# Performance work log

Hardware: AMD Instinct MI355X
Metric: run time of the kernel (lower is better)

Reference implementation:

```python
import jax, jax.numpy as jnp
import numpy as np


def setup_inputs() -> dict:
    key = jax.random.key(0)
    ks = jax.random.split(key, 4)
    B, T, D, H, E = 4, 2048, 1024, 4096, 8
    s = 0.02
    x = jax.random.normal(ks[0], (B, T, D), dtype=jnp.float32)
    Wr = jax.random.normal(ks[1], (D, E), dtype=jnp.float32) * s
    br = jnp.zeros((E,), dtype=jnp.float32)
    W1 = jax.random.normal(ks[2], (E, D, H), dtype=jnp.float32) * s
    b1 = jnp.zeros((E, H), dtype=jnp.float32)
    W2 = jax.random.normal(ks[3], (E, H, D), dtype=jnp.float32) * s
    b2 = jnp.zeros((E, D), dtype=jnp.float32)
    return {"x": x, "Wr": Wr, "br": br, "W1": W1, "b1": b1, "W2": W2, "b2": b2}


def reference(x, Wr, br, W1, b1, W2, b2):
    # Router: top-1 selection
    logits = jnp.einsum('btd,de->bte', x, Wr) + br            # [B,T,E]
    probs = jax.nn.softmax(logits, axis=-1)                   # [B,T,E]
    expert_idx = jnp.argmax(probs, axis=-1)                   # [B,T] int
    E = W1.shape[0]
    onehot = jax.nn.one_hot(expert_idx, E, dtype=x.dtype)     # [B,T,E]
    # Dense grouped-MLP over all experts, then combine with one-hot routing.
    # h: [B,E,T,H]
    h = jax.nn.relu(jnp.einsum('btd,edh->beth', x, W1) + b1[None, :, None, :])
    y = jnp.einsum('beth,ehd->betd', h, W2) + b2[None, :, None, :]  # [B,E,T,D]
    out = jnp.einsum('bte,betd->btd', onehot, y)              # [B,T,D]
    return out, probs, expert_idx
```

## Files before the change

kernel.cpp:

```cpp
#include <hip/hip_runtime.h>

#define NTOK 8192
#define DD 1024
#define HH 4096
#define EE 8
#define MAXBLK 72

typedef __attribute__((ext_vector_type(8))) short bf16x8;
typedef __attribute__((ext_vector_type(4))) float f32x4;

__device__ __forceinline__ unsigned short f2bf(float f) {
  unsigned u = __builtin_bit_cast(unsigned, f);
  u += 0x7fffu + ((u >> 16) & 1u);
  return (unsigned short)(u >> 16);
}

union Pack8 {
  unsigned short u[8];
  uint4 v;
};

__device__ __forceinline__ void gload_lds16(const void* g, void* l) {
  __builtin_amdgcn_global_load_lds(
      (const __attribute__((address_space(1))) unsigned int*)g,
      (__attribute__((address_space(3))) unsigned int*)l, 16, 0, 0);
}

__global__ __launch_bounds__(256) void k_router(
    const float* __restrict__ x, const float* __restrict__ Wr,
    const float* __restrict__ br, float* __restrict__ probs,
    float* __restrict__ idxf, int* __restrict__ idxi) {
  const int lane = threadIdx.x & 63;
  const int token = blockIdx.x * 4 + (threadIdx.x >> 6);
  const float* xr = x + (size_t)token * DD;

  float acc[EE];
#pragma unroll
  for (int e = 0; e < EE; ++e) acc[e] = 0.f;

#pragma unroll
  for (int i = 0; i < 4; ++i) {
    const int d0 = i * 256 + lane * 4;
    const float4 xv = *reinterpret_cast<const float4*>(xr + d0);
    const float xs[4] = {xv.x, xv.y, xv.z, xv.w};
#pragma unroll
    for (int j = 0; j < 4; ++j) {
      const float xd = xs[j];
      const float4 w0 = *reinterpret_cast<const float4*>(Wr + (size_t)(d0 + j) * EE);
      const float4 w1 = *reinterpret_cast<const float4*>(Wr + (size_t)(d0 + j) * EE + 4);
      acc[0] += xd * w0.x; acc[1] += xd * w0.y; acc[2] += xd * w0.z; acc[3] += xd * w0.w;
      acc[4] += xd * w1.x; acc[5] += xd * w1.y; acc[6] += xd * w1.z; acc[7] += xd * w1.w;
    }
  }
#pragma unroll
  for (int s = 32; s > 0; s >>= 1) {
#pragma unroll
    for (int e = 0; e < EE; ++e) acc[e] += __shfl_xor(acc[e], s, 64);
  }

  float lg[EE];
#pragma unroll
  for (int e = 0; e < EE; ++e) lg[e] = acc[e] + br[e];

  int best = 0;
  float bv = lg[0];
#pragma unroll
  for (int e = 1; e < EE; ++e) {
    if (lg[e] > bv) { bv = lg[e]; best = e; }
  }
  float p[EE], s = 0.f;
#pragma unroll
  for (int e = 0; e < EE; ++e) { p[e] = expf(lg[e] - bv); s += p[e]; }
  const float inv = 1.f / s;

  if (lane == 0) {
#pragma unroll
    for (int e = 0; e < EE; ++e) probs[(size_t)token * EE + e] = p[e] * inv;
    idxf[token] = (float)best;
    idxi[token] = best;
  }
}

__global__ __launch_bounds__(512) void k_compact(const int* __restrict__ idxi,
                                                 int* __restrict__ cnt,
                                                 int* __restrict__ off,
                                                 int* __restrict__ sorted,
                                                 int* __restrict__ meta) {
  __shared__ int sidx[NTOK];
  __shared__ int scnt[EE], soff[EE];
  const int tid = threadIdx.x;
  for (int i = tid; i < NTOK; i += 512) sidx[i] = idxi[i];
  __syncthreads();
  const int w = tid >> 6, lane = tid & 63;
  if (w < EE) {
    int c = 0;
    for (int i = 0; i < NTOK / 64; ++i) {
      unsigned long long m = __ballot(sidx[i * 64 + lane] == w);
      c += __popcll(m);
    }
    if (lane == 0) scnt[w] = c;
  }
  __syncthreads();
  if (tid == 0) {
    int s = 0;
    for (int e = 0; e < EE; ++e) { soff[e] = s; s += scnt[e]; }
    int nb = 0;
    for (int e = 0; e < EE; ++e) {
      const int nmb = (scnt[e] + 127) >> 7;
      for (int m = 0; m < nmb; ++m) {
        meta[16 + nb] = e;
        meta[96 + nb] = m << 7;
        ++nb;
      }
    }
    meta[0] = nb;
  }
  __syncthreads();
  if (w < EE) {
    int base = soff[w];
    const unsigned long long ltmask = (1ull << lane) - 1ull;
    for (int i = 0; i < NTOK / 64; ++i) {
      const int tok = i * 64 + lane;
      const bool f = (sidx[tok] == w);
      unsigned long long m = __ballot(f);
      if (f) {
        int r = __popcll(m & ltmask);
        sorted[base + r] = tok;
      }
      base += __popcll(m);
    }
    if (lane == 0) { cnt[w] = scnt[w]; off[w] = soff[w]; }
  }
}

__global__ __launch_bounds__(256) void k_cvt_x(const float* __restrict__ x,
                                               unsigned short* __restrict__ xb) {
  const size_t i = ((size_t)blockIdx.x * 256 + threadIdx.x) * 8;
  const float4 a = *reinterpret_cast<const float4*>(x + i);
  const float4 b = *reinterpret_cast<const float4*>(x + i + 4);
  Pack8 p;
  p.u[0] = f2bf(a.x); p.u[1] = f2bf(a.y); p.u[2] = f2bf(a.z); p.u[3] = f2bf(a.w);
  p.u[4] = f2bf(b.x); p.u[5] = f2bf(b.y); p.u[6] = f2bf(b.z); p.u[7] = f2bf(b.w);
  *reinterpret_cast<uint4*>(xb + i) = p.v;
}

__global__ __launch_bounds__(256) void k_trcvt(const float* __restrict__ in,
                                               unsigned short* __restrict__ outp,
                                               int R, int C) {
  const int e = blockIdx.z;
  const float* src = in + (size_t)e * R * C;
  unsigned short* dst = outp + (size_t)e * R * C;
  __shared__ float t[32][33];
  const int r0 = blockIdx.y * 32, c0 = blockIdx.x * 32;
  const int tr = threadIdx.x >> 3, tc4 = (threadIdx.x & 7) * 4;
  const float4 v = *reinterpret_cast<const float4*>(src + (size_t)(r0 + tr) * C + c0 + tc4);
  t[tr][tc4 + 0] = v.x; t[tr][tc4 + 1] = v.y; t[tr][tc4 + 2] = v.z; t[tr][tc4 + 3] = v.w;
  __syncthreads();
  union { unsigned short u[4]; uint2 v2; } p;
#pragma unroll
  for (int j = 0; j < 4; ++j) p.u[j] = f2bf(t[tc4 + j][tr]);
  *reinterpret_cast<uint2*>(&dst[(size_t)(c0 + tr) * R + r0 + tc4]) = p.v2;
}

__global__ __launch_bounds__(256) void k_gemm1n(
    const unsigned short* __restrict__ xb, const unsigned short* __restrict__ W1t,
    const float* __restrict__ b1, const int* __restrict__ meta,
    const int* __restrict__ cnt, const int* __restrict__ off,
    const int* __restrict__ sorted, unsigned short* __restrict__ h) {
  const int bid = blockIdx.x;
  if (bid >= meta[0]) return;
  const int e = meta[16 + bid];
  const int m0 = meta[96 + bid];
  const int c = cnt[e], base = off[e];
  const int n0 = blockIdx.y * 128;

  __shared__ __align__(16) unsigned short Al[128 * 64];
  __shared__ __align__(16) unsigned short Bl[128 * 64];

  const int tid = threadIdx.x, l = tid & 63, w = tid >> 6;

  const unsigned short* aptr[4];
  const unsigned short* bptr[4];
  unsigned short* alds[4];
  unsigned short* blds[4];
#pragma unroll
  for (int i = 0; i < 4; ++i) {
    const int r = i * 32 + w * 8 + (l >> 3);
    const int swz = ((l & 7) ^ (r & 7)) * 8;
    int ar = m0 + r; if (ar >= c) ar = c - 1;
    const int tok = sorted[base + ar];
    aptr[i] = xb + (size_t)tok * DD + swz;
    bptr[i] = W1t + ((size_t)e * HH + n0 + r) * DD + swz;
    alds[i] = &Al[r * 64 + (l & 7) * 8];
    blds[i] = &Bl[r * 64 + (l & 7) * 8];
  }

  const int lr = l & 15, lg = l >> 4;
  const int wr = w >> 1, wc = w & 1;
  int aoff[4], bofr[4], aswz[4], bswz[4];
#pragma unroll
  for (int m = 0; m < 4; ++m) {
    int row = wr * 64 + m * 16 + lr;
    aoff[m] = row * 64; aswz[m] = row & 7;
    row = wc * 64 + m * 16 + lr;
    bofr[m] = row * 64; bswz[m] = row & 7;
  }

  f32x4 acc[4][4];
#pragma unroll
  for (int m = 0; m < 4; ++m)
#pragma unroll
    for (int n = 0; n < 4; ++n) acc[m][n] = {0.f, 0.f, 0.f, 0.f};

  for (int k0 = 0; k0 < DD; k0 += 64) {
    __syncthreads();
#pragma unroll
    for (int i = 0; i < 4; ++i) gload_lds16(aptr[i] + k0, alds[i]);
#pragma unroll
    for (int i = 0; i < 4; ++i) gload_lds16(bptr[i] + k0, blds[i]);
    __syncthreads();
#pragma unroll
    for (int ks = 0; ks < 2; ++ks) {
      bf16x8 af[4], bv[4];
#pragma unroll
      for (int m = 0; m < 4; ++m)
        af[m] = *reinterpret_cast<const bf16x8*>(&Al[aoff[m] + (((ks * 4 + lg) ^ aswz[m]) * 8)]);
#pragma unroll
      for (int n = 0; n < 4; ++n)
        bv[n] = *reinterpret_cast<const bf16x8*>(&Bl[bofr[n] + (((ks * 4 + lg) ^ bswz[n]) * 8)]);
#pragma unroll
      for (int m = 0; m < 4; ++m)
#pragma unroll
        for (int n = 0; n < 4; ++n)
          acc[m][n] = __builtin_amdgcn_mfma_f32_16x16x32_bf16(af[m], bv[n], acc[m][n], 0, 0, 0);
    }
  }

  const int valid = c - m0;
#pragma unroll
  for (int m = 0; m < 4; ++m) {
#pragma unroll
    for (int rr = 0; rr < 4; ++rr) {
      const int tr = wr * 64 + m * 16 + lg * 4 + rr;
      if (tr < valid) {
        const size_t row = (size_t)(base + m0 + tr);
#pragma unroll
        for (int n = 0; n < 4; ++n) {
          const int col = n0 + wc * 64 + n * 16 + lr;
          const float v = acc[m][n][rr] + b1[e * HH + col];
          h[row * HH + col] = f2bf(fmaxf(v, 0.f));
        }
      }
    }
  }
}

__global__ __launch_bounds__(256) void k_gemm2n(
    const unsigned short* __restrict__ h, const unsigned short* __restrict__ W2t,
    const float* __restrict__ b2, const int* __restrict__ meta,
    const int* __restrict__ cnt, const int* __restrict__ off,
    const int* __restrict__ sorted, float* __restrict__ out) {
  const int bid = blockIdx.x;
  if (bid >= meta[0]) return;
  const int e = meta[16 + bid];
  const int m0 = meta[96 + bid];
  const int c = cnt[e], base = off[e];
  const int n0 = blockIdx.y * 128;

  __shared__ __align__(16) unsigned short Al[128 * 64];
  __shared__ __align__(16) unsigned short Bl[128 * 64];

  const int tid = threadIdx.x, l = tid & 63, w = tid >> 6;

  const unsigned short* aptr[4];
  const unsigned short* bptr[4];
  unsigned short* alds[4];
  unsigned short* blds[4];
#pragma unroll
  for (int i = 0; i < 4; ++i) {
    const int r = i * 32 + w * 8 + (l >> 3);
    const int swz = ((l & 7) ^ (r & 7)) * 8;
    int ar = m0 + r; if (ar >= c) ar = c - 1;
    aptr[i] = h + (size_t)(base + ar) * HH + swz;
    bptr[i] = W2t + ((size_t)e * DD + n0 + r) * HH + swz;
    alds[i] = &Al[r * 64 + (l & 7) * 8];
    blds[i] = &Bl[r * 64 + (l & 7) * 8];
  }

  const int lr = l & 15, lg = l >> 4;
  const int wr = w >> 1, wc = w & 1;
  int aoff[4], bofr[4], aswz[4], bswz[4];
#pragma unroll
  for (int m = 0; m < 4; ++m) {
    int row = wr * 64 + m * 16 + lr;
    aoff[m] = row * 64; aswz[m] = row & 7;
    row = wc * 64 + m * 16 + lr;
    bofr[m] = row * 64; bswz[m] = row & 7;
  }

  f32x4 acc[4][4];
#pragma unroll
  for (int m = 0; m < 4; ++m)
#pragma unroll
    for (int n = 0; n < 4; ++n) acc[m][n] = {0.f, 0.f, 0.f, 0.f};

  for (int k0 = 0; k0 < HH; k0 += 64) {
    __syncthreads();
#pragma unroll
    for (int i = 0; i < 4; ++i) gload_lds16(aptr[i] + k0, alds[i]);
#pragma unroll
    for (int i = 0; i < 4; ++i) gload_lds16(bptr[i] + k0, blds[i]);
    __syncthreads();
#pragma unroll
    for (int ks = 0; ks < 2; ++ks) {
      bf16x8 af[4], bv[4];
#pragma unroll
      for (int m = 0; m < 4; ++m)
        af[m] = *reinterpret_cast<const bf16x8*>(&Al[aoff[m] + (((ks * 4 + lg) ^ aswz[m]) * 8)]);
#pragma unroll
      for (int n = 0; n < 4; ++n)
        bv[n] = *reinterpret_cast<const bf16x8*>(&Bl[bofr[n] + (((ks * 4 + lg) ^ bswz[n]) * 8)]);
#pragma unroll
      for (int m = 0; m < 4; ++m)
#pragma unroll
        for (int n = 0; n < 4; ++n)
          acc[m][n] = __builtin_amdgcn_mfma_f32_16x16x32_bf16(af[m], bv[n], acc[m][n], 0, 0, 0);
    }
  }

  const int valid = c - m0;
#pragma unroll
  for (int m = 0; m < 4; ++m) {
#pragma unroll
    for (int rr = 0; rr < 4; ++rr) {
      const int tr = wr * 64 + m * 16 + lg * 4 + rr;
      if (tr < valid) {
        const int token = sorted[base + m0 + tr];
#pragma unroll
        for (int n = 0; n < 4; ++n) {
          const int col = n0 + wc * 64 + n * 16 + lr;
          out[(size_t)token * DD + col] = acc[m][n][rr] + b2[e * DD + col];
        }
      }
    }
  }
}

#define BM 128
#define BN 128
#define BK 32
#define PAD 40

__global__ __launch_bounds__(256) void k_gemm1_f32(
    const float* __restrict__ x, const float* __restrict__ W1,
    const float* __restrict__ b1, const int* __restrict__ cnt,
    const int* __restrict__ off, const int* __restrict__ sorted,
    unsigned short* __restrict__ h) {
  const int e = blockIdx.x >> 6;
  const int mb = blockIdx.x & 63;
  const int n0 = blockIdx.y * BN;
  const int c = cnt[e];
  const int m0 = mb * BM;
  if (m0 >= c) return;
  const int base = off[e];

  __shared__ __align__(16) unsigned short Al[BM * PAD];
  __shared__ __align__(16) unsigned short Bl[BN * PAD];

  const int tid = threadIdx.x;
  const int ar = tid >> 1, ah = tid & 1;
  int arow = m0 + ar; if (arow >= c) arow = c - 1;
  const int atok = sorted[base + arow];
  const float* asrc = x + (size_t)atok * DD + ah * 16;
  const int bn = tid & 127, bkg = tid >> 7;
  const float* bsrc = W1 + (size_t)e * DD * HH + (size_t)(bkg * 16) * HH + n0 + bn;

  const int lane = tid & 63, w = tid >> 6;
  const int wr = w >> 1, wc = w & 1;
  const int lr = lane & 15, lg = lane >> 4;

  f32x4 acc[4][4];
#pragma unroll
  for (int m = 0; m < 4; ++m)
#pragma unroll
    for (int n = 0; n < 4; ++n) acc[m][n] = {0.f, 0.f, 0.f, 0.f};

  for (int k0 = 0; k0 < DD; k0 += BK) {
    Pack8 pa0, pa1;
    {
      const float* s4 = asrc + k0;
#pragma unroll
      for (int q = 0; q < 2; ++q) {
        float4 f = *reinterpret_cast<const float4*>(s4 + q * 4);
        pa0.u[q * 4 + 0] = f2bf(f.x); pa0.u[q * 4 + 1] = f2bf(f.y);
        pa0.u[q * 4 + 2] = f2bf(f.z); pa0.u[q * 4 + 3] = f2bf(f.w);
      }
#pragma unroll
      for (int q = 0; q < 2; ++q) {
        float4 f = *reinterpret_cast<const float4*>(s4 + 8 + q * 4);
        pa1.u[q * 4 + 0] = f2bf(f.x); pa1.u[q * 4 + 1] = f2bf(f.y);
        pa1.u[q * 4 + 2] = f2bf(f.z); pa1.u[q * 4 + 3] = f2bf(f.w);
      }
    }
    Pack8 pb0, pb1;
    {
      const float* bs = bsrc + (size_t)k0 * HH;
#pragma unroll
      for (int q = 0; q < 8; ++q) pb0.u[q] = f2bf(bs[(size_t)q * HH]);
#pragma unroll
      for (int q = 0; q < 8; ++q) pb1.u[q] = f2bf(bs[(size_t)(q + 8) * HH]);
    }
    __syncthreads();
    *reinterpret_cast<uint4*>(&Al[ar * PAD + ah * 16]) = pa0.v;
    *reinterpret_cast<uint4*>(&Al[ar * PAD + ah * 16 + 8]) = pa1.v;
    *reinterpret_cast<uint4*>(&Bl[bn * PAD + bkg * 16]) = pb0.v;
    *reinterpret_cast<uint4*>(&Bl[bn * PAD + bkg * 16 + 8]) = pb1.v;
    __syncthreads();

    bf16x8 af[4], bf[4];
#pragma unroll
    for (int m = 0; m < 4; ++m)
      af[m] = *reinterpret_cast<const bf16x8*>(&Al[(wr * 64 + m * 16 + lr) * PAD + lg * 8]);
#pragma unroll
    for (int n = 0; n < 4; ++n)
      bf[n] = *reinterpret_cast<const bf16x8*>(&Bl[(wc * 64 + n * 16 + lr) * PAD + lg * 8]);
#pragma unroll
    for (int m = 0; m < 4; ++m)
#pragma unroll
      for (int n = 0; n < 4; ++n)
        acc[m][n] = __builtin_amdgcn_mfma_f32_16x16x32_bf16(af[m], bf[n], acc[m][n], 0, 0, 0);
  }

  const int valid = c - m0;
#pragma unroll
  for (int m = 0; m < 4; ++m) {
#pragma unroll
    for (int r = 0; r < 4; ++r) {
      const int tr = wr * 64 + m * 16 + lg * 4 + r;
      if (tr < valid) {
        const size_t row = (size_t)(base + m0 + tr);
#pragma unroll
        for (int n = 0; n < 4; ++n) {
          const int col = n0 + wc * 64 + n * 16 + lr;
          float v = acc[m][n][r] + b1[e * HH + col];
          v = fmaxf(v, 0.f);
          h[row * HH + col] = f2bf(v);
        }
      }
    }
  }
}

__global__ __launch_bounds__(256) void k_gemm2_f32(
    const unsigned short* __restrict__ h, const float* __restrict__ W2,
    const float* __restrict__ b2, const int* __restrict__ cnt,
    const int* __restrict__ off, const int* __restrict__ sorted,
    float* __restrict__ out) {
  const int e = blockIdx.x >> 6;
  const int mb = blockIdx.x & 63;
  const int n0 = blockIdx.y * BN;
  const int c = cnt[e];
  const int m0 = mb * BM;
  if (m0 >= c) return;
  const int base = off[e];

  __shared__ __align__(16) unsigned short Al[BM * PAD];
  __shared__ __align__(16) unsigned short Bl[BN * PAD];

  const int tid = threadIdx.x;
  const int ar = tid >> 1, ah = tid & 1;
  int arow = m0 + ar; if (arow >= c) arow = c - 1;
  const unsigned short* asrc = h + (size_t)(base + arow) * HH + ah * 16;
  const int bn = tid & 127, bkg = tid >> 7;
  const float* bsrc = W2 + (size_t)e * HH * DD + (size_t)(bkg * 16) * DD + n0 + bn;

  const int lane = tid & 63, w = tid >> 6;
  const int wr = w >> 1, wc = w & 1;
  const int lr = lane & 15, lg = lane >> 4;

  f32x4 acc[4][4];
#pragma unroll
  for (int m = 0; m < 4; ++m)
#pragma unroll
    for (int n = 0; n < 4; ++n) acc[m][n] = {0.f, 0.f, 0.f, 0.f};

  for (int k0 = 0; k0 < HH; k0 += BK) {
    const uint4 a0 = *reinterpret_cast<const uint4*>(asrc + k0);
    const uint4 a1 = *reinterpret_cast<const uint4*>(asrc + k0 + 8);
    Pack8 pb0, pb1;
    {
      const float* bs = bsrc + (size_t)k0 * DD;
#pragma unroll
      for (int q = 0; q < 8; ++q) pb0.u[q] = f2bf(bs[(size_t)q * DD]);
#pragma unroll
      for (int q = 0; q < 8; ++q) pb1.u[q] = f2bf(bs[(size_t)(q + 8) * DD]);
    }
    __syncthreads();
    *reinterpret_cast<uint4*>(&Al[ar * PAD + ah * 16]) = a0;
    *reinterpret_cast<uint4*>(&Al[ar * PAD + ah * 16 + 8]) = a1;
    *reinterpret_cast<uint4*>(&Bl[bn * PAD + bkg * 16]) = pb0.v;
    *reinterpret_cast<uint4*>(&Bl[bn * PAD + bkg * 16 + 8]) = pb1.v;
    __syncthreads();

    bf16x8 af[4], bf[4];
#pragma unroll
    for (int m = 0; m < 4; ++m)
      af[m] = *reinterpret_cast<const bf16x8*>(&Al[(wr * 64 + m * 16 + lr) * PAD + lg * 8]);
#pragma unroll
    for (int n = 0; n < 4; ++n)
      bf[n] = *reinterpret_cast<const bf16x8*>(&Bl[(wc * 64 + n * 16 + lr) * PAD + lg * 8]);
#pragma unroll
    for (int m = 0; m < 4; ++m)
#pragma unroll
      for (int n = 0; n < 4; ++n)
        acc[m][n] = __builtin_amdgcn_mfma_f32_16x16x32_bf16(af[m], bf[n], acc[m][n], 0, 0, 0);
  }

  const int valid = c - m0;
#pragma unroll
  for (int m = 0; m < 4; ++m) {
#pragma unroll
    for (int r = 0; r < 4; ++r) {
      const int tr = wr * 64 + m * 16 + lg * 4 + r;
      if (tr < valid) {
        const int token = sorted[base + m0 + tr];
#pragma unroll
        for (int n = 0; n < 4; ++n) {
          const int col = n0 + wc * 64 + n * 16 + lr;
          out[(size_t)token * DD + col] = acc[m][n][r] + b2[e * DD + col];
        }
      }
    }
  }
}

extern "C" void kernel_launch(void* const* d_in, const int* in_sizes, int n_in,
                              void* d_out, int out_size, void* d_ws, size_t ws_size,
                              hipStream_t stream) {
  const float* x  = (const float*)d_in[0];
  const float* Wr = (const float*)d_in[1];
  const float* br = (const float*)d_in[2];
  const float* W1 = (const float*)d_in[3];
  const float* b1 = (const float*)d_in[4];
  const float* W2 = (const float*)d_in[5];
  const float* b2 = (const float*)d_in[6];

  float* out   = (float*)d_out;
  float* probs = out + (size_t)NTOK * DD;
  float* idxf  = probs + (size_t)NTOK * EE;

  char* ws = (char*)d_ws;
  int* cnt    = (int*)(ws + 0);
  int* off    = (int*)(ws + 64);
  int* meta   = (int*)(ws + 128);
  int* idxi   = (int*)(ws + 1024);
  int* sorted = (int*)(ws + 33792);

  const size_t OFF_XB  = 66560;
  const size_t OFF_W1T = OFF_XB + (size_t)NTOK * DD * 2;
  const size_t OFF_H   = OFF_W1T + (size_t)EE * DD * HH * 2;
  const size_t OFF_W2T = OFF_XB;
  const size_t NEED    = OFF_H + (size_t)NTOK * HH * 2;

  k_router<<<NTOK / 4, 256, 0, stream>>>(x, Wr, br, probs, idxf, idxi);
  k_compact<<<1, 512, 0, stream>>>(idxi, cnt, off, sorted, meta);

  if (ws_size >= NEED) {
    unsigned short* xb  = (unsigned short*)(ws + OFF_XB);
    unsigned short* W1t = (unsigned short*)(ws + OFF_W1T);
    unsigned short* W2t = (unsigned short*)(ws + OFF_W2T);
    unsigned short* h   = (unsigned short*)(ws + OFF_H);
    k_cvt_x<<<(NTOK * DD) / (256 * 8), 256, 0, stream>>>(x, xb);
    k_trcvt<<<dim3(HH / 32, DD / 32, EE), 256, 0, stream>>>(W1, W1t, DD, HH);
    k_gemm1n<<<dim3(MAXBLK, HH / 128), 256, 0, stream>>>(xb, W1t, b1, meta, cnt, off, sorted, h);
    k_trcvt<<<dim3(DD / 32, HH / 32, EE), 256, 0, stream>>>(W2, W2t, HH, DD);
    k_gemm2n<<<dim3(MAXBLK, DD / 128), 256, 0, stream>>>(h, W2t, b2, meta, cnt, off, sorted, out);
  } else {
    unsigned short* h = (unsigned short*)(ws + OFF_XB);
    k_gemm1_f32<<<dim3(EE * (NTOK / BM), HH / BN), 256, 0, stream>>>(x, W1, b1, cnt, off, sorted, h);
    k_gemm2_f32<<<dim3(EE * (NTOK / BM), DD / BN), 256, 0, stream>>>(h, W2, b2, cnt, off, sorted, out);
  }
}
```

Baseline: 400.7 us.

## Double-buffer GEMM LDS tiles, fuse x conversion into router, widen transpose tiles

Both grouped GEMMs now keep two LDS buffers and prefetch the next K-tile with global_load_lds while computing on the current one. Barriers use manual vmcnt waits so the global-load latency can overlap with MFMA work. The bf16 conversion of x moves into the router kernel, removing a separate pass over x, and the weight transpose-convert now uses 64x64 tiles that store bf16 in LDS and write 16-byte rows. The fp32 fallback path and its workspace-size check are removed, so the code assumes the workspace is large enough, and doubling LDS may lower occupancy.

```diff
diff --git a/kernel.cpp b/kernel.cpp
--- a/kernel.cpp
+++ b/kernel.cpp
@@ -5,6 +5,8 @@
 #define HH 4096
 #define EE 8
 #define MAXBLK 72
+#define NT1 16
+#define NT2 64
 
 typedef __attribute__((ext_vector_type(8))) short bf16x8;
 typedef __attribute__((ext_vector_type(4))) float f32x4;
@@ -29,7 +31,8 @@
 __global__ __launch_bounds__(256) void k_router(
     const float* __restrict__ x, const float* __restrict__ Wr,
     const float* __restrict__ br, float* __restrict__ probs,
-    float* __restrict__ idxf, int* __restrict__ idxi) {
+    float* __restrict__ idxf, int* __restrict__ idxi,
+    unsigned short* __restrict__ xb) {
   const int lane = threadIdx.x & 63;
   const int token = blockIdx.x * 4 + (threadIdx.x >> 6);
   const float* xr = x + (size_t)token * DD;
@@ -42,6 +45,10 @@
   for (int i = 0; i < 4; ++i) {
     const int d0 = i * 256 + lane * 4;
     const float4 xv = *reinterpret_cast<const float4*>(xr + d0);
+    union { unsigned short u[4]; uint2 v; } pk;
+    pk.u[0] = f2bf(xv.x); pk.u[1] = f2bf(xv.y);
+    pk.u[2] = f2bf(xv.z); pk.u[3] = f2bf(xv.w);
+    *reinterpret_cast<uint2*>(xb + (size_t)token * DD + d0) = pk.v;
     const float xs[4] = {xv.x, xv.y, xv.z, xv.w};
 #pragma unroll
     for (int j = 0; j < 4; ++j) {
@@ -133,33 +140,33 @@
   }
 }
 
-__global__ __launch_bounds__(256) void k_cvt_x(const float* __restrict__ x,
-                                               unsigned short* __restrict__ xb) {
-  const size_t i = ((size_t)blockIdx.x * 256 + threadIdx.x) * 8;
-  const float4 a = *reinterpret_cast<const float4*>(x + i);
-  const float4 b = *reinterpret_cast<const float4*>(x + i + 4);
-  Pack8 p;
-  p.u[0] = f2bf(a.x); p.u[1] = f2bf(a.y); p.u[2] = f2bf(a.z); p.u[3] = f2bf(a.w);
-  p.u[4] = f2bf(b.x); p.u[5] = f2bf(b.y); p.u[6] = f2bf(b.z); p.u[7] = f2bf(b.w);
-  *reinterpret_cast<uint4*>(xb + i) = p.v;
-}
-
-__global__ __launch_bounds__(256) void k_trcvt(const float* __restrict__ in,
-                                               unsigned short* __restrict__ outp,
-                                               int R, int C) {
+__global__ __launch_bounds__(256) void k_trcvt64(const float* __restrict__ in,
+                                                 unsigned short* __restrict__ outp,
+                                                 int R, int C) {
   const int e = blockIdx.z;
-  const float* src = in + (size_t)e * R * C;
-  unsigned short* dst = outp + (size_t)e * R * C;
-  __shared__ float t[32][33];
-  const int r0 = blockIdx.y * 32, c0 = blockIdx.x * 32;
-  const int tr = threadIdx.x >> 3, tc4 = (threadIdx.x & 7) * 4;
-  const float4 v = *reinterpret_cast<const float4*>(src + (size_t)(r0 + tr) * C + c0 + tc4);
-  t[tr][tc4 + 0] = v.x; t[tr][tc4 + 1] = v.y; t[tr][tc4 + 2] = v.z; t[tr][tc4 + 3] = v.w;
+  const int r0 = blockIdx.y * 64, c0 = blockIdx.x * 64;
+  const float* src = in + (size_t)e * R * C + (size_t)r0 * C + c0;
+  unsigned short* dst = outp + (size_t)e * R * C + (size_t)c0 * R + r0;
+  __shared__ unsigned short t[64 * 66];
+  const int tid = threadIdx.x;
+#pragma unroll
+  for (int it = 0; it < 4; ++it) {
+    const int r = it * 16 + (tid >> 4), c4 = (tid & 15) * 4;
+    const float4 v = *reinterpret_cast<const float4*>(src + (size_t)r * C + c4);
+    t[r * 66 + c4 + 0] = f2bf(v.x);
+    t[r * 66 + c4 + 1] = f2bf(v.y);
+    t[r * 66 + c4 + 2] = f2bf(v.z);
+    t[r * 66 + c4 + 3] = f2bf(v.w);
+  }
   __syncthreads();
-  union { unsigned short u[4]; uint2 v2; } p;
-#pragma unroll
-  for (int j = 0; j < 4; ++j) p.u[j] = f2bf(t[tc4 + j][tr]);
-  *reinterpret_cast<uint2*>(&dst[(size_t)(c0 + tr) * R + r0 + tc4]) = p.v2;
+#pragma unroll
+  for (int it = 0; it < 2; ++it) {
+    const int cc = it * 32 + (tid >> 3), r8 = (tid & 7) * 8;
+    Pack8 p;
+#pragma unroll
+    for (int j = 0; j < 8; ++j) p.u[j] = t[(r8 + j) * 66 + cc];
+    *reinterpret_cast<uint4*>(dst + (size_t)cc * R + r8) = p.v;
+  }
 }
 
 __global__ __launch_bounds__(256) void k_gemm1n(
@@ -174,15 +181,14 @@
   const int c = cnt[e], base = off[e];
   const int n0 = blockIdx.y * 128;
 
-  __shared__ __align__(16) unsigned short Al[128 * 64];
-  __shared__ __align__(16) unsigned short Bl[128 * 64];
+  __shared__ __align__(16) unsigned short Al[2][128 * 64];
+  __shared__ __align__(16) unsigned short Bl[2][128 * 64];
 
   const int tid = threadIdx.x, l = tid & 63, w = tid >> 6;
 
   const unsigned short* aptr[4];
   const unsigned short* bptr[4];
-  unsigned short* alds[4];
-  unsigned short* blds[4];
+  int soff4[4];
 #pragma unroll
   for (int i = 0; i < 4; ++i) {
     const int r = i * 32 + w * 8 + (l >> 3);
@@ -191,19 +197,18 @@
     const int tok = sorted[base + ar];
     aptr[i] = xb + (size_t)tok * DD + swz;
     bptr[i] = W1t + ((size_t)e * HH + n0 + r) * DD + swz;
-    alds[i] = &Al[r * 64 + (l & 7) * 8];
-    blds[i] = &Bl[r * 64 + (l & 7) * 8];
+    soff4[i] = r * 64 + (l & 7) * 8;
   }
 
   const int lr = l & 15, lg = l >> 4;
   const int wr = w >> 1, wc = w & 1;
-  int aoff[4], bofr[4], aswz[4], bswz[4];
+  int aoff[4], boff[4], asw[4], bsw[4];
 #pragma unroll
   for (int m = 0; m < 4; ++m) {
     int row = wr * 64 + m * 16 + lr;
-    aoff[m] = row * 64; aswz[m] = row & 7;
+    aoff[m] = row * 64; asw[m] = row & 7;
     row = wc * 64 + m * 16 + lr;
-    bofr[m] = row * 64; bswz[m] = row & 7;
+    boff[m] = row * 64; bsw[m] = row & 7;
   }
 
   f32x4 acc[4][4];
@@ -212,28 +217,68 @@
 #pragma unroll
     for (int n = 0; n < 4; ++n) acc[m][n] = {0.f, 0.f, 0.f, 0.f};
 
-  for (int k0 = 0; k0 < DD; k0 += 64) {
-    __syncthreads();
-#pragma unroll
-    for (int i = 0; i < 4; ++i) gload_lds16(aptr[i] + k0, alds[i]);
-#pragma unroll
-    for (int i = 0; i < 4; ++i) gload_lds16(bptr[i] + k0, blds[i]);
-    __syncthreads();
-#pragma unroll
-    for (int ks = 0; ks < 2; ++ks) {
+#pragma unroll
+  for (int i = 0; i < 4; ++i) gload_lds16(aptr[i], &Al[0][soff4[i]]);
+#pragma unroll
+  for (int i = 0; i < 4; ++i) gload_lds16(bptr[i], &Bl[0][soff4[i]]);
+
+  int cur = 0;
+#pragma unroll 1
+  for (int t = 0; t < NT1 - 1; ++t) {
+    const int kn = (t + 1) * 64;
+#pragma unroll
+    for (int i = 0; i < 4; ++i) gload_lds16(aptr[i] + kn, &Al[cur ^ 1][soff4[i]]);
+    asm volatile("s_waitcnt vmcnt(4)" ::: "memory");
+    __builtin_amdgcn_s_barrier();
+    {
       bf16x8 af[4], bv[4];
 #pragma unroll
       for (int m = 0; m < 4; ++m)
-        af[m] = *reinterpret_cast<const bf16x8*>(&Al[aoff[m] + (((ks * 4 + lg) ^ aswz[m]) * 8)]);
-#pragma unroll
-      for (int n = 0; n < 4; ++n)
-        bv[n] = *reinterpret_cast<const bf16x8*>(&Bl[bofr[n] + (((ks * 4 + lg) ^ bswz[n]) * 8)]);
+        af[m] = *reinterpret_cast<const bf16x8*>(&Al[cur][aoff[m] + ((lg ^ asw[m]) * 8)]);
+#pragma unroll
+      for (int n = 0; n < 4; ++n)
+        bv[n] = *reinterpret_cast<const bf16x8*>(&Bl[cur][boff[n] + ((lg ^ bsw[n]) * 8)]);
 #pragma unroll
       for (int m = 0; m < 4; ++m)
 #pragma unroll
         for (int n = 0; n < 4; ++n)
           acc[m][n] = __builtin_amdgcn_mfma_f32_16x16x32_bf16(af[m], bv[n], acc[m][n], 0, 0, 0);
     }
+#pragma unroll
+    for (int i = 0; i < 4; ++i) gload_lds16(bptr[i] + kn, &Bl[cur ^ 1][soff4[i]]);
+    {
+      bf16x8 af[4], bv[4];
+#pragma unroll
+      for (int m = 0; m < 4; ++m)
+        af[m] = *reinterpret_cast<const bf16x8*>(&Al[cur][aoff[m] + (((4 + lg) ^ asw[m]) * 8)]);
+#pragma unroll
+      for (int n = 0; n < 4; ++n)
+        bv[n] = *reinterpret_cast<const bf16x8*>(&Bl[cur][boff[n] + (((4 + lg) ^ bsw[n]) * 8)]);
+#pragma unroll
+      for (int m = 0; m < 4; ++m)
+#pragma unroll
+        for (int n = 0; n < 4; ++n)
+          acc[m][n] = __builtin_amdgcn_mfma_f32_16x16x32_bf16(af[m], bv[n], acc[m][n], 0, 0, 0);
+    }
+    __builtin_amdgcn_s_barrier();
+    cur ^= 1;
+  }
+  asm volatile("s_waitcnt vmcnt(0)" ::: "memory");
+  __builtin_amdgcn_s_barrier();
+#pragma unroll
+  for (int ks = 0; ks < 2; ++ks) {
+    bf16x8 af[4], bv[4];
+#pragma unroll
+    for (int m = 0; m < 4; ++m)
+      af[m] = *reinterpret_cast<const bf16x8*>(&Al[cur][aoff[m] + (((ks * 4 + lg) ^ asw[m]) * 8)]);
+#pragma unroll
+    for (int n = 0; n < 4; ++n)
+      bv[n] = *reinterpret_cast<const bf16x8*>(&Bl[cur][boff[n] + (((ks * 4 + lg) ^ bsw[n]) * 8)]);
+#pragma unroll
+    for (int m = 0; m < 4; ++m)
+#pragma unroll
+      for (int n = 0; n < 4; ++n)
+        acc[m][n] = __builtin_amdgcn_mfma_f32_16x16x32_bf16(af[m], bv[n], acc[m][n], 0, 0, 0);
   }
 
   const int valid = c - m0;
@@ -267,15 +312,14 @@
   const int c = cnt[e], base = off[e];
   const int n0 = blockIdx.y * 128;
 
-  __shared__ __align__(16) unsigned short Al[128 * 64];
-  __shared__ __align__(16) unsigned short Bl[128 * 64];
+  __shared__ __align__(16) unsigned short Al[2][128 * 64];
+  __shared__ __align__(16) unsigned short Bl[2][128 * 64];
 
   const int tid = threadIdx.x, l = tid & 63, w = tid >> 6;
 
   const unsigned short* aptr[4];
   const unsigned short* bptr[4];
-  unsigned short* alds[4];
-  unsigned short* blds[4];
+  int soff4[4];
 #pragma unroll
   for (int i = 0; i < 4; ++i) {
     const int r = i * 32 + w * 8 + (l >> 3);
@@ -283,19 +327,18 @@
     int ar = m0 + r; if (ar >= c) ar = c - 1;
     aptr[i] = h + (size_t)(base + ar) * HH + swz;
     bptr[i] = W2t + ((size_t)e * DD + n0 + r) * HH + swz;
-    alds[i] = &Al[r * 64 + (l & 7) * 8];
-    blds[i] = &Bl[r * 64 + (l & 7) * 8];
+    soff4[i] = r * 64 + (l & 7) * 8;
   }
 
   const int lr = l & 15, lg = l >> 4;
   const int wr = w >> 1, wc = w & 1;
-  int aoff[4], bofr[4], aswz[4], bswz[4];
+  int aoff[4], boff[4], asw[4], bsw[4];
 #pragma unroll
   for (int m = 0; m < 4; ++m) {
     int row = wr * 64 + m * 16 + lr;
-    aoff[m] = row * 64; aswz[m] = row & 7;
+    aoff[m] = row * 64; asw[m] = row & 7;
     row = wc * 64 + m * 16 + lr;
-    bofr[m] = row * 64; bswz[m] = row & 7;
+    boff[m] = row * 64; bsw[m] = row & 7;
   }
 
   f32x4 acc[4][4];
@@ -304,28 +347,68 @@
 #pragma unroll
     for (int n = 0; n < 4; ++n) acc[m][n] = {0.f, 0.f, 0.f, 0.f};
 
-  for (int k0 = 0; k0 < HH; k0 += 64) {
-    __syncthreads();
-#pragma unroll
-    for (int i = 0; i < 4; ++i) gload_lds16(aptr[i] + k0, alds[i]);
-#pragma unroll
-    for (int i = 0; i < 4; ++i) gload_lds16(bptr[i] + k0, blds[i]);
-    __syncthreads();
-#pragma unroll
-    for (int ks = 0; ks < 2; ++ks) {
+#pragma unroll
+  for (int i = 0; i < 4; ++i) gload_lds16(aptr[i], &Al[0][soff4[i]]);
+#pragma unroll
+  for (int i = 0; i < 4; ++i) gload_lds16(bptr[i], &Bl[0][soff4[i]]);
+
+  int cur = 0;
+#pragma unroll 1
+  for (int t = 0; t < NT2 - 1; ++t) {
+    const int kn = (t + 1) * 64;
+#pragma unroll
+    for (int i = 0; i < 4; ++i) gload_lds16(aptr[i] + kn, &Al[cur ^ 1][soff4[i]]);
+    asm volatile("s_waitcnt vmcnt(4)" ::: "memory");
+    __builtin_amdgcn_s_barrier();
+    {
       bf16x8 af[4], bv[4];
 #pragma unroll
       for (int m = 0; m < 4; ++m)
-        af[m] = *reinterpret_cast<const bf16x8*>(&Al[aoff[m] + (((ks * 4 + lg) ^ aswz[m]) * 8)]);
-#pragma unroll
-      for (int n = 0; n < 4; ++n)
-        bv[n] = *reinterpret_cast<const bf16x8*>(&Bl[bofr[n] + (((ks * 4 + lg) ^ bswz[n]) * 8)]);
+        af[m] = *reinterpret_cast<const bf16x8*>(&Al[cur][aoff[m] + ((lg ^ asw[m]) * 8)]);
+#pragma unroll
+      for (int n = 0; n < 4; ++n)
+        bv[n] = *reinterpret_cast<const bf16x8*>(&Bl[cur][boff[n] + ((lg ^ bsw[n]) * 8)]);
 #pragma unroll
       for (int m = 0; m < 4; ++m)
 #pragma unroll
         for (int n = 0; n < 4; ++n)
           acc[m][n] = __builtin_amdgcn_mfma_f32_16x16x32_bf16(af[m], bv[n], acc[m][n], 0, 0, 0);
     }
+#pragma unroll
+    for (int i = 0; i < 4; ++i) gload_lds16(bptr[i] + kn, &Bl[cur ^ 1][soff4[i]]);
+    {
+      bf16x8 af[4], bv[4];
+#pragma unroll
+      for (int m = 0; m < 4; ++m)
+        af[m] = *reinterpret_cast<const bf16x8*>(&Al[cur][aoff[m] + (((4 + lg) ^ asw[m]) * 8)]);
+#pragma unroll
+      for (int n = 0; n < 4; ++n)
+        bv[n] = *reinterpret_cast<const bf16x8*>(&Bl[cur][boff[n] + (((4 + lg) ^ bsw[n]) * 8)]);
+#pragma unroll
+      for (int m = 0; m < 4; ++m)
+#pragma unroll
+        for (int n = 0; n < 4; ++n)
+          acc[m][n] = __builtin_amdgcn_mfma_f32_16x16x32_bf16(af[m], bv[n], acc[m][n], 0, 0, 0);
+    }
+    __builtin_amdgcn_s_barrier();
+    cur ^= 1;
+  }
+  asm volatile("s_waitcnt vmcnt(0)" ::: "memory");
+  __builtin_amdgcn_s_barrier();
+#pragma unroll
+  for (int ks = 0; ks < 2; ++ks) {
+    bf16x8 af[4], bv[4];
+#pragma unroll
+    for (int m = 0; m < 4; ++m)
+      af[m] = *reinterpret_cast<const bf16x8*>(&Al[cur][aoff[m] + (((ks * 4 + lg) ^ asw[m]) * 8)]);
+#pragma unroll
+    for (int n = 0; n < 4; ++n)
+      bv[n] = *reinterpret_cast<const bf16x8*>(&Bl[cur][boff[n] + (((ks * 4 + lg) ^ bsw[n]) * 8)]);
+#pragma unroll
+    for (int m = 0; m < 4; ++m)
+#pragma unroll
+      for (int n = 0; n < 4; ++n)
+        acc[m][n] = __builtin_amdgcn_mfma_f32_16x16x32_bf16(af[m], bv[n], acc[m][n], 0, 0, 0);
   }
 
   const int valid = c - m0;
@@ -340,194 +423,6 @@
         for (int n = 0; n < 4; ++n) {
           const int col = n0 + wc * 64 + n * 16 + lr;
           out[(size_t)token * DD + col] = acc[m][n][rr] + b2[e * DD + col];
-        }
-      }
-    }
-  }
-}
-
-#define BM 128
-#define BN 128
-#define BK 32
-#define PAD 40
-
-__global__ __launch_bounds__(256) void k_gemm1_f32(
-    const float* __restrict__ x, const float* __restrict__ W1,
-    const float* __restrict__ b1, const int* __restrict__ cnt,
-    const int* __restrict__ off, const int* __restrict__ sorted,
-    unsigned short* __restrict__ h) {
-  const int e = blockIdx.x >> 6;
-  const int mb = blockIdx.x & 63;
-  const int n0 = blockIdx.y * BN;
-  const int c = cnt[e];
-  const int m0 = mb * BM;
-  if (m0 >= c) return;
-  const int base = off[e];
-
-  __shared__ __align__(16) unsigned short Al[BM * PAD];
-  __shared__ __align__(16) unsigned short Bl[BN * PAD];
-
-  const int tid = threadIdx.x;
-  const int ar = tid >> 1, ah = tid & 1;
-  int arow = m0 + ar; if (arow >= c) arow = c - 1;
-  const int atok = sorted[base + arow];
-  const float* asrc = x + (size_t)atok * DD + ah * 16;
-  const int bn = tid & 127, bkg = tid >> 7;
-  const float* bsrc = W1 + (size_t)e * DD * HH + (size_t)(bkg * 16) * HH + n0 + bn;
-
-  const int lane = tid & 63, w = tid >> 6;
-  const int wr = w >> 1, wc = w & 1;
-  const int lr = lane & 15, lg = lane >> 4;
-
-  f32x4 acc[4][4];
-#pragma unroll
-  for (int m = 0; m < 4; ++m)
-#pragma unroll
-    for (int n = 0; n < 4; ++n) acc[m][n] = {0.f, 0.f, 0.f, 0.f};
-
-  for (int k0 = 0; k0 < DD; k0 += BK) {
-    Pack8 pa0, pa1;
-    {
-      const float* s4 = asrc + k0;
-#pragma unroll
-      for (int q = 0; q < 2; ++q) {
-        float4 f = *reinterpret_cast<const float4*>(s4 + q * 4);
-        pa0.u[q * 4 + 0] = f2bf(f.x); pa0.u[q * 4 + 1] = f2bf(f.y);
-        pa0.u[q * 4 + 2] = f2bf(f.z); pa0.u[q * 4 + 3] = f2bf(f.w);
-      }
-#pragma unroll
-      for (int q = 0; q < 2; ++q) {
-        float4 f = *reinterpret_cast<const float4*>(s4 + 8 + q * 4);
-        pa1.u[q * 4 + 0] = f2bf(f.x); pa1.u[q * 4 + 1] = f2bf(f.y);
-        pa1.u[q * 4 + 2] = f2bf(f.z); pa1.u[q * 4 + 3] = f2bf(f.w);
-      }
-    }
-    Pack8 pb0, pb1;
-    {
-      const float* bs = bsrc + (size_t)k0 * HH;
-#pragma unroll
-      for (int q = 0; q < 8; ++q) pb0.u[q] = f2bf(bs[(size_t)q * HH]);
-#pragma unroll
-      for (int q = 0; q < 8; ++q) pb1.u[q] = f2bf(bs[(size_t)(q + 8) * HH]);
-    }
-    __syncthreads();
-    *reinterpret_cast<uint4*>(&Al[ar * PAD + ah * 16]) = pa0.v;
-    *reinterpret_cast<uint4*>(&Al[ar * PAD + ah * 16 + 8]) = pa1.v;
-    *reinterpret_cast<uint4*>(&Bl[bn * PAD + bkg * 16]) = pb0.v;
-    *reinterpret_cast<uint4*>(&Bl[bn * PAD + bkg * 16 + 8]) = pb1.v;
-    __syncthreads();
-
-    bf16x8 af[4], bf[4];
-#pragma unroll
-    for (int m = 0; m < 4; ++m)
-      af[m] = *reinterpret_cast<const bf16x8*>(&Al[(wr * 64 + m * 16 + lr) * PAD + lg * 8]);
-#pragma unroll
-    for (int n = 0; n < 4; ++n)
-      bf[n] = *reinterpret_cast<const bf16x8*>(&Bl[(wc * 64 + n * 16 + lr) * PAD + lg * 8]);
-#pragma unroll
-    for (int m = 0; m < 4; ++m)
-#pragma unroll
-      for (int n = 0; n < 4; ++n)
-        acc[m][n] = __builtin_amdgcn_mfma_f32_16x16x32_bf16(af[m], bf[n], acc[m][n], 0, 0, 0);
-  }
-
-  const int valid = c - m0;
-#pragma unroll
-  for (int m = 0; m < 4; ++m) {
-#pragma unroll
-    for (int r = 0; r < 4; ++r) {
-      const int tr = wr * 64 + m * 16 + lg * 4 + r;
-      if (tr < valid) {
-        const size_t row = (size_t)(base + m0 + tr);
-#pragma unroll
-        for (int n = 0; n < 4; ++n) {
-          const int col = n0 + wc * 64 + n * 16 + lr;
-          float v = acc[m][n][r] + b1[e * HH + col];
-          v = fmaxf(v, 0.f);
-          h[row * HH + col] = f2bf(v);
-        }
-      }
-    }
-  }
-}
-
-__global__ __launch_bounds__(256) void k_gemm2_f32(
-    const unsigned short* __restrict__ h, const float* __restrict__ W2,
-    const float* __restrict__ b2, const int* __restrict__ cnt,
-    const int* __restrict__ off, const int* __restrict__ sorted,
-    float* __restrict__ out) {
-  const int e = blockIdx.x >> 6;
-  const int mb = blockIdx.x & 63;
-  const int n0 = blockIdx.y * BN;
-  const int c = cnt[e];
-  const int m0 = mb * BM;
-  if (m0 >= c) return;
-  const int base = off[e];
-
-  __shared__ __align__(16) unsigned short Al[BM * PAD];
-  __shared__ __align__(16) unsigned short Bl[BN * PAD];
-
-  const int tid = threadIdx.x;
-  const int ar = tid >> 1, ah = tid & 1;
-  int arow = m0 + ar; if (arow >= c) arow = c - 1;
-  const unsigned short* asrc = h + (size_t)(base + arow) * HH + ah * 16;
-  const int bn = tid & 127, bkg = tid >> 7;
-  const float* bsrc = W2 + (size_t)e * HH * DD + (size_t)(bkg * 16) * DD + n0 + bn;
-
-  const int lane = tid & 63, w = tid >> 6;
-  const int wr = w >> 1, wc = w & 1;
-  const int lr = lane & 15, lg = lane >> 4;
-
-  f32x4 acc[4][4];
-#pragma unroll
-  for (int m = 0; m < 4; ++m)
-#pragma unroll
-    for (int n = 0; n < 4; ++n) acc[m][n] = {0.f, 0.f, 0.f, 0.f};
-
-  for (int k0 = 0; k0 < HH; k0 += BK) {
-    const uint4 a0 = *reinterpret_cast<const uint4*>(asrc + k0);
-    const uint4 a1 = *reinterpret_cast<const uint4*>(asrc + k0 + 8);
-    Pack8 pb0, pb1;
-    {
-      const float* bs = bsrc + (size_t)k0 * DD;
-#pragma unroll
-      for (int q = 0; q < 8; ++q) pb0.u[q] = f2bf(bs[(size_t)q * DD]);
-#pragma unroll
-      for (int q = 0; q < 8; ++q) pb1.u[q] = f2bf(bs[(size_t)(q + 8) * DD]);
-    }
-    __syncthreads();
-    *reinterpret_cast<uint4*>(&Al[ar * PAD + ah * 16]) = a0;
-    *reinterpret_cast<uint4*>(&Al[ar * PAD + ah * 16 + 8]) = a1;
-    *reinterpret_cast<uint4*>(&Bl[bn * PAD + bkg * 16]) = pb0.v;
-    *reinterpret_cast<uint4*>(&Bl[bn * PAD + bkg * 16 + 8]) = pb1.v;
-    __syncthreads();
-
-    bf16x8 af[4], bf[4];
-#pragma unroll
-    for (int m = 0; m < 4; ++m)
-      af[m] = *reinterpret_cast<const bf16x8*>(&Al[(wr * 64 + m * 16 + lr) * PAD + lg * 8]);
-#pragma unroll
-    for (int n = 0; n < 4; ++n)
-      bf[n] = *reinterpret_cast<const bf16x8*>(&Bl[(wc * 64 + n * 16 + lr) * PAD + lg * 8]);
-#pragma unroll
-    for (int m = 0; m < 4; ++m)
-#pragma unroll
-      for (int n = 0; n < 4; ++n)
-        acc[m][n] = __builtin_amdgcn_mfma_f32_16x16x32_bf16(af[m], bf[n], acc[m][n], 0, 0, 0);
-  }
-
-  const int valid = c - m0;
-#pragma unroll
-  for (int m = 0; m < 4; ++m) {
-#pragma unroll
-    for (int r = 0; r < 4; ++r) {
-      const int tr = wr * 64 + m * 16 + lg * 4 + r;
-      if (tr < valid) {
-        const int token = sorted[base + m0 + tr];
-#pragma unroll
-        for (int n = 0; n < 4; ++n) {
-          const int col = n0 + wc * 64 + n * 16 + lr;
-          out[(size_t)token * DD + col] = acc[m][n][r] + b2[e * DD + col];
         }
       }
     }
@@ -560,24 +455,16 @@
   const size_t OFF_W1T = OFF_XB + (size_t)NTOK * DD * 2;
   const size_t OFF_H   = OFF_W1T + (size_t)EE * DD * HH * 2;
   const size_t OFF_W2T = OFF_XB;
-  const size_t NEED    = OFF_H + (size_t)NTOK * HH * 2;
-
-  k_router<<<NTOK / 4, 256, 0, stream>>>(x, Wr, br, probs, idxf, idxi);
+
+  unsigned short* xb  = (unsigned short*)(ws + OFF_XB);
+  unsigned short* W1t = (unsigned short*)(ws + OFF_W1T);
+  unsigned short* W2t = (unsigned short*)(ws + OFF_W2T);
+  unsigned short* h   = (unsigned short*)(ws + OFF_H);
+
+  k_router<<<NTOK / 4, 256, 0, stream>>>(x, Wr, br, probs, idxf, idxi, xb);
   k_compact<<<1, 512, 0, stream>>>(idxi, cnt, off, sorted, meta);
-
-  if (ws_size >= NEED) {
-    unsigned short* xb  = (unsigned short*)(ws + OFF_XB);
-    unsigned short* W1t = (unsigned short*)(ws + OFF_W1T);
-    unsigned short* W2t = (unsigned short*)(ws + OFF_W2T);
-    unsigned short* h   = (unsigned short*)(ws + OFF_H);
-    k_cvt_x<<<(NTOK * DD) / (256 * 8), 256, 0, stream>>>(x, xb);
-    k_trcvt<<<dim3(HH / 32, DD / 32, EE), 256, 0, stream>>>(W1, W1t, DD, HH);
-    k_gemm1n<<<dim3(MAXBLK, HH / 128), 256, 0, stream>>>(xb, W1t, b1, meta, cnt, off, sorted, h);
-    k_trcvt<<<dim3(DD / 32, HH / 32, EE), 256, 0, stream>>>(W2, W2t, HH, DD);
-    k_gemm2n<<<dim3(MAXBLK, DD / 128), 256, 0, stream>>>(h, W2t, b2, meta, cnt, off, sorted, out);
-  } else {
-    unsigned short* h = (unsigned short*)(ws + OFF_XB);
-    k_gemm1_f32<<<dim3(EE * (NTOK / BM), HH / BN), 256, 0, stream>>>(x, W1, b1, cnt, off, sorted, h);
-    k_gemm2_f32<<<dim3(EE * (NTOK / BM), DD / BN), 256, 0, stream>>>(h, W2, b2, cnt, off, sorted, out);
-  }
-}
+  k_trcvt64<<<dim3(HH / 64, DD / 64, EE), 256, 0, stream>>>(W1, W1t, DD, HH);
+  k_gemm1n<<<dim3(MAXBLK, HH / 128), 256, 0, stream>>>(xb, W1t, b1, meta, cnt, off, sorted, h);
+  k_trcvt64<<<dim3(DD / 64, HH / 64, EE), 256, 0, stream>>>(W2, W2t, HH, DD);
+  k_gemm2n<<<dim3(MAXBLK, DD / 128), 256, 0, stream>>>(h, W2t, b2, meta, cnt, off, sorted, out);
+}
```

Measured after the change: 412.0 us. 1.03x slower.
